# Kernel optimization log

Hardware: AMD Instinct MI355X
Metric: run time of the kernel (lower is better)

The kernel has to match this reference:

```python
import jax, jax.numpy as jnp
import numpy as np

N = 12288

def setup_inputs() -> dict:
    key = jax.random.key(0)
    k1, k2, k3 = jax.random.split(key, 3)
    params = jax.random.normal(k1, (N,), dtype=jnp.float32)
    r_mask = jax.random.randint(k2, (N,), 0, 2, dtype=jnp.int32)
    ics_mask = jax.random.randint(k3, (N,), 0, 2, dtype=jnp.int32)
    return {"params": params, "r_mask": r_mask, "ics_mask": ics_mask}

def reference(params, r_mask, ics_mask):
    # Original: -diag(params) @ diag(r_mask).float() + diag(ics_mask)
    # Mathematically: diag(ics_mask - params * r_mask), an [N, N] matrix.
    diag_vals = ics_mask.astype(params.dtype) - params * r_mask.astype(params.dtype)
    return jnp.diag(diag_vals)
```

## Files before the change

### kernel.cpp

```cpp
#include <hip/hip_runtime.h>


#define DIAG_N 12288
#define DIAG_N4 (DIAG_N / 4)

__global__ __launch_bounds__(256) void diag_fill_kernel(
    const float* __restrict__ params,
    const int*   __restrict__ r_mask,
    const int*   __restrict__ ics_mask,
    float4*      __restrict__ out)
{
    const int total4 = DIAG_N * DIAG_N4;
    const int stride = gridDim.x * blockDim.x;
    for (int idx = blockIdx.x * blockDim.x + threadIdx.x;
         idx < total4; idx += stride) {
        const int row = idx / DIAG_N4;
        const int rem = idx - row * DIAG_N4;
        float4 v = make_float4(0.f, 0.f, 0.f, 0.f);
        if (rem == (row >> 2)) {
            const float d = (float)ics_mask[row]
                          - params[row] * (float)r_mask[row];
            const int lane = row & 3;
            v.x = (lane == 0) ? d : 0.f;
            v.y = (lane == 1) ? d : 0.f;
            v.z = (lane == 2) ? d : 0.f;
            v.w = (lane == 3) ? d : 0.f;
        }
        out[idx] = v;
    }
}

extern "C" void kernel_launch(void* const* d_in, const int* in_sizes, int n_in,
                              void* d_out, int out_size, void* d_ws, size_t ws_size,
                              hipStream_t stream) {
    const float* params   = (const float*)d_in[0];
    const int*   r_mask   = (const int*)d_in[1];
    const int*   ics_mask = (const int*)d_in[2];
    float4*      out      = (float4*)d_out;

    dim3 grid(2048), block(256);
    hipLaunchKernelGGL(diag_fill_kernel, grid, block, 0, stream,
                       params, r_mask, ics_mask, out);
}
```

Before: 595.0 us.

## Zero output with hipMemsetAsync and scatter only diagonal elements

Replaces the grid-stride kernel, which wrote every float4 of the N×N output and computed indices per element, with a driver memset that zero-fills the buffer plus a small kernel that writes only the N diagonal values. The aim is to use the runtime's tuned fill path for the bulk zero writes and remove the per-element divide and compare work. This adds a second operation on the stream, and it assumes out_size counts float elements.

New measurement: 572.4 us. 3.8% less time.

```diff
diff --git a/kernel.cpp b/kernel.cpp
--- a/kernel.cpp
+++ b/kernel.cpp
@@ -2,31 +2,17 @@
 
 
 #define DIAG_N 12288
-#define DIAG_N4 (DIAG_N / 4)
 
-__global__ __launch_bounds__(256) void diag_fill_kernel(
+__global__ __launch_bounds__(256) void diag_scatter_kernel(
     const float* __restrict__ params,
     const int*   __restrict__ r_mask,
     const int*   __restrict__ ics_mask,
-    float4*      __restrict__ out)
+    float*       __restrict__ out)
 {
-    const int total4 = DIAG_N * DIAG_N4;
-    const int stride = gridDim.x * blockDim.x;
-    for (int idx = blockIdx.x * blockDim.x + threadIdx.x;
-         idx < total4; idx += stride) {
-        const int row = idx / DIAG_N4;
-        const int rem = idx - row * DIAG_N4;
-        float4 v = make_float4(0.f, 0.f, 0.f, 0.f);
-        if (rem == (row >> 2)) {
-            const float d = (float)ics_mask[row]
-                          - params[row] * (float)r_mask[row];
-            const int lane = row & 3;
-            v.x = (lane == 0) ? d : 0.f;
-            v.y = (lane == 1) ? d : 0.f;
-            v.z = (lane == 2) ? d : 0.f;
-            v.w = (lane == 3) ? d : 0.f;
-        }
-        out[idx] = v;
+    const int i = blockIdx.x * blockDim.x + threadIdx.x;
+    if (i < DIAG_N) {
+        const float d = (float)ics_mask[i] - params[i] * (float)r_mask[i];
+        out[(size_t)i * (DIAG_N + 1)] = d;
     }
 }
 
@@ -36,9 +22,11 @@
     const float* params   = (const float*)d_in[0];
     const int*   r_mask   = (const int*)d_in[1];
     const int*   ics_mask = (const int*)d_in[2];
-    float4*      out      = (float4*)d_out;
+    float*       out      = (float*)d_out;
 
-    dim3 grid(2048), block(256);
-    hipLaunchKernelGGL(diag_fill_kernel, grid, block, 0, stream,
+    hipMemsetAsync(d_out, 0, (size_t)out_size * sizeof(float), stream);
+
+    dim3 grid((DIAG_N + 255) / 256), block(256);
+    hipLaunchKernelGGL(diag_scatter_kernel, grid, block, 0, stream,
                        params, r_mask, ics_mask, out);
 }
```
